# Kernel tuning notes

Hardware: AMD Instinct MI355X
Metric: run time of the kernel (lower is better)

The kernel has to match this reference:

```python
import jax, jax.numpy as jnp
import numpy as np

N, E, G = 50000, 600000, 50
IN_CH, HID, OUT, HEADS = 5, 64, 32, 4
BN_EPS = 1e-5


def setup_inputs() -> dict:
    key = jax.random.key(0)
    ks = jax.random.split(key, 32)

    def p(i, shape, scale=0.1):
        return jax.random.normal(ks[i], shape, dtype=jnp.float32) * scale

    inp = {
        "x": jax.random.normal(ks[0], (N, IN_CH), dtype=jnp.float32),
        "edge_index": jax.random.randint(ks[1], (2, E), 0, N),
        "batch": jnp.sort(jax.random.randint(ks[2], (N,), 0, G)),
        "enc_w": p(3, (IN_CH, HID)),
        "enc_b": jnp.zeros((HID,), jnp.float32),
    }
    dims = [(HID, HID), (HID, HID), (HID, OUT)]
    i = 4
    for l, (din, dout) in enumerate(dims):
        inp[f"w{l}"] = p(i, (din, HEADS * dout)); i += 1
        inp[f"as{l}"] = p(i, (HEADS, dout)); i += 1
        inp[f"ad{l}"] = p(i, (HEADS, dout)); i += 1
        inp[f"b{l}"] = jnp.zeros((dout,), jnp.float32)
        inp[f"g{l}"] = jnp.ones((dout,), jnp.float32)
        inp[f"be{l}"] = jnp.zeros((dout,), jnp.float32)
    for name in ("eth", "man"):
        inp[f"{name}_w1"] = p(i, (OUT, OUT // 2)); i += 1
        inp[f"{name}_b1"] = jnp.zeros((OUT // 2,), jnp.float32)
        inp[f"{name}_w2"] = p(i, (OUT // 2, 1)); i += 1
        inp[f"{name}_b2"] = jnp.zeros((1,), jnp.float32)
    return inp


def _gat(h_in, src, dst, W, a_s, a_d, bias, dout):
    # PyG GATConv, heads=HEADS, concat=False (mean over heads)
    h = (h_in @ W).reshape(N, HEADS, dout)          # [N,H,C]
    es = (h * a_s).sum(-1)                          # [N,H] src attention term
    ed = (h * a_d).sum(-1)                          # [N,H] dst attention term
    e = jax.nn.leaky_relu(es[src] + ed[dst], 0.2)   # [E,H]
    m = jax.ops.segment_max(e, dst, num_segments=N)
    ex = jnp.exp(e - m[dst])
    s = jax.ops.segment_sum(ex, dst, num_segments=N)
    alpha = ex / (s[dst] + 1e-16)                   # edge softmax per dst
    out = jax.ops.segment_sum(h[src] * alpha[..., None], dst, num_segments=N)
    return out.mean(axis=1) + bias                  # mean over heads + bias


def _bn(x, g, b):  # BatchNorm1d with batch statistics
    mu = x.mean(0)
    var = x.var(0)
    return g * (x - mu) * jax.lax.rsqrt(var + BN_EPS) + b


def _head(g, w1, b1, w2, b2):
    return jax.nn.sigmoid(jax.nn.relu(g @ w1 + b1) @ w2 + b2)


def reference(x, edge_index, batch, enc_w, enc_b,
              w0, as0, ad0, b0, g0, be0,
              w1, as1, ad1, b1, g1, be1,
              w2, as2, ad2, b2, g2, be2,
              eth_w1, eth_b1, eth_w2, eth_b2,
              man_w1, man_b1, man_w2, man_b2):
    loops = jnp.arange(N)
    src = jnp.concatenate([edge_index[0], loops])
    dst = jnp.concatenate([edge_index[1], loops])

    h = x @ enc_w + enc_b
    layers = [(w0, as0, ad0, b0, g0, be0, HID),
              (w1, as1, ad1, b1, g1, be1, HID),
              (w2, as2, ad2, b2, g2, be2, OUT)]
    for i, (W, a_s, a_d, bias, gm, bt, dout) in enumerate(layers):
        h = _gat(h, src, dst, W, a_s, a_d, bias, dout)
        h = _bn(h, gm, bt)
        if i < len(layers) - 1:
            h = jax.nn.relu(h)  # dropout is identity at inference

    ones = jnp.ones((N,), h.dtype)
    counts = jax.ops.segment_sum(ones, batch, num_segments=G)  # [G]
    gsum = jax.ops.segment_sum(h, batch, num_segments=G)
    gmean = gsum / jnp.maximum(counts, 1.0)[:, None]
    gmax = jax.ops.segment_max(h, batch, num_segments=G)
    gmax = jnp.where(counts[:, None] > 0, gmax, 0.0)
    gemb = (gmean + gmax + gsum) / 3.0

    ethics = _head(gemb, eth_w1, eth_b1, eth_w2, eth_b2)
    manip = _head(gemb, man_w1, man_b1, man_w2, man_b2)
    return h, gemb, ethics, manip
```

## Files before the change

kernel.cpp:

```cpp
#include <hip/hip_runtime.h>
#include <math.h>

constexpr int kN  = 50000;
constexpr int kE  = 600000;
constexpr int kET = 650000;
constexpr int kG  = 50;
constexpr int kH  = 4;
constexpr int kRep = 16;

constexpr size_t OFF_HCUR   = 0;
constexpr size_t OFF_HNEXT  = 1600000;
constexpr size_t OFF_Z      = 4800000;
constexpr size_t OFF_ES     = 11200000;
constexpr size_t OFF_ED     = 11400000;
constexpr size_t OFF_ROWPTR = 14200000;
constexpr size_t OFF_SRC    = 14320000;
constexpr size_t OFF_WT2    = 14970000;
constexpr size_t OFF_AHAT   = 15000000;
constexpr size_t OFF_SPART  = 15002000;
constexpr size_t OFF_CURSOR = 15010000;
constexpr size_t OFF_BNREP  = 15060000;
constexpr size_t OFF_GPOOL  = 15066144;
constexpr size_t kZeroEnd   = 15069344;

constexpr int kScanBlocks = (kN + 1023) / 1024;
constexpr int kHistBlocks = (kET + 255) / 256;
constexpr int kPrepBlocks = 163;
constexpr int kEncBlocks  = kN / 4;

typedef __bf16 bf16x8 __attribute__((ext_vector_type(8)));
typedef float  f32x4  __attribute__((ext_vector_type(4)));

__device__ inline ushort f2b(float f) {
    unsigned u = __float_as_uint(f);
    return (ushort)((u + 0x7FFFu + ((u >> 16) & 1u)) >> 16);
}
__device__ inline float b2f(ushort u) {
    return __uint_as_float(((unsigned)u) << 16);
}
__device__ inline unsigned enc_f(float f) {
    unsigned b = __float_as_uint(f);
    return (b & 0x80000000u) ? ~b : (b | 0x80000000u);
}
__device__ inline float dec_f(unsigned u) {
    return __uint_as_float((u & 0x80000000u) ? (u & 0x7FFFFFFFu) : ~u);
}

__device__ inline void edge_pair(const int* __restrict__ ei, int e, int& src, int& dst) {
    if (e < kE) { src = ei[e]; dst = ei[kE + e]; }
    else        { src = e - kE; dst = e - kE; }
}

__global__ void k_histprep(const int* __restrict__ ei, int* __restrict__ counts,
                           const float* __restrict__ w0, const float* __restrict__ w1,
                           const float* __restrict__ w2, const float* __restrict__ as0,
                           const float* __restrict__ as1, const float* __restrict__ as2,
                           const float* __restrict__ ad0, const float* __restrict__ ad1,
                           const float* __restrict__ ad2, float* __restrict__ ahat,
                           ushort* __restrict__ Wt2) {
    int b = blockIdx.x;
    if (b < 3) {
        const float* W  = (b == 0) ? w0 : (b == 1) ? w1 : w2;
        const float* As = (b == 0) ? as0 : (b == 1) ? as1 : as2;
        const float* Ad = (b == 0) ? ad0 : (b == 1) ? ad1 : ad2;
        int dout = (b == 2) ? 32 : 64;
        int i = threadIdx.x;
        int h = i >> 6, k = i & 63;
        const float* wr = W + (size_t)k * (4 * dout) + h * dout;
        float s1 = 0.f, s2 = 0.f;
        for (int c = 0; c < dout; ++c) {
            float w = wr[c];
            s1 += w * As[h * dout + c];
            s2 += w * Ad[h * dout + c];
        }
        ahat[b * 512 + i] = s1;
        ahat[b * 512 + 256 + i] = s2;
    } else if (b < kPrepBlocks) {
        int i = (b - 3) * 256 + threadIdx.x;
        if (i >= 40960) return;
        int l, li;
        if (i < 16384)      { l = 0; li = i; }
        else if (i < 32768) { l = 1; li = i - 16384; }
        else                { l = 2; li = i - 32768; }
        int dout = (l == 2) ? 32 : 64;
        const float* W = (l == 0) ? w0 : (l == 1) ? w1 : w2;
        int c = li >> 8, kk = li & 255;
        int h = kk >> 6, k = kk & 63;
        Wt2[l * 16384 + li] = f2b(W[(size_t)k * (4 * dout) + h * dout + c]);
    } else {
        int e = (b - kPrepBlocks) * 256 + threadIdx.x;
        if (e >= kET) return;
        int src, dst;
        edge_pair(ei, e, src, dst);
        atomicAdd(&counts[dst], 1);
    }
}

__global__ void __launch_bounds__(1024) k_scan_local(const int* __restrict__ counts,
                                                     int* __restrict__ rowptr,
                                                     int* __restrict__ partials) {
    int tid = threadIdx.x;
    int idx = blockIdx.x * 1024 + tid;
    int val = (idx < kN) ? counts[idx] : 0;
    int lane = tid & 63, w = tid >> 6;
    int x = val;
#pragma unroll
    for (int off = 1; off < 64; off <<= 1) {
        int t = __shfl_up(x, off);
        if (lane >= off) x += t;
    }
    __shared__ int wsum[16];
    if (lane == 63) wsum[w] = x;
    __syncthreads();
    if (w == 0 && lane < 16) {
        int y = wsum[lane];
#pragma unroll
        for (int off = 1; off < 16; off <<= 1) {
            int t = __shfl_up(y, off);
            if (lane >= off) y += t;
        }
        wsum[lane] = y;
    }
    __syncthreads();
    int incl = x + (w > 0 ? wsum[w - 1] : 0);
    if (idx < kN) rowptr[idx + 1] = incl;
    if (tid == 1023) partials[blockIdx.x] = incl;
}

__global__ void k_scan_part(int* __restrict__ partials) {
    int lane = threadIdx.x;
    int v = (lane < kScanBlocks) ? partials[lane] : 0;
    int x = v;
#pragma unroll
    for (int off = 1; off < 64; off <<= 1) {
        int t = __shfl_up(x, off);
        if (lane >= off) x += t;
    }
    if (lane < kScanBlocks) partials[lane] = x - v;
}

__global__ void __launch_bounds__(1024) k_scan_add(int* __restrict__ cursor,
                                                   int* __restrict__ rowptr,
                                                   const int* __restrict__ partials) {
    int idx = blockIdx.x * 1024 + threadIdx.x;
    if (idx >= kN) return;
    int incl = rowptr[idx + 1] + partials[blockIdx.x];
    rowptr[idx + 1] = incl;
    int val = cursor[idx];
    cursor[idx] = incl - val;
    if (idx == 0) rowptr[0] = 0;
}

__global__ void __launch_bounds__(256) k_scatter_enc(const int* __restrict__ ei,
                                                     int* __restrict__ cursor,
                                                     int* __restrict__ src_csr,
                                                     const float* __restrict__ x,
                                                     const float* __restrict__ w,
                                                     const float* __restrict__ b,
                                                     const float* __restrict__ ahat0,
                                                     ushort* __restrict__ h,
                                                     float* __restrict__ es,
                                                     float* __restrict__ ed) {
    if (blockIdx.x < kEncBlocks) {
        int node = blockIdx.x * 4 + (threadIdx.x >> 6);
        int lane = threadIdx.x & 63;
        float acc = b[lane];
#pragma unroll
        for (int k = 0; k < 5; ++k) acc += x[node * 5 + k] * w[k * 64 + lane];
        h[(size_t)node * 64 + lane] = f2b(acc);

        float ps[4], pd[4];
#pragma unroll
        for (int hh = 0; hh < 4; ++hh) {
            ps[hh] = acc * ahat0[hh * 64 + lane];
            pd[hh] = acc * ahat0[256 + hh * 64 + lane];
        }
#pragma unroll
        for (int off = 1; off < 64; off <<= 1) {
#pragma unroll
            for (int hh = 0; hh < 4; ++hh) {
                ps[hh] += __shfl_xor(ps[hh], off);
                pd[hh] += __shfl_xor(pd[hh], off);
            }
        }
        if (lane == 0) {
            ((float4*)es)[node] = make_float4(ps[0], ps[1], ps[2], ps[3]);
            ((float4*)ed)[node] = make_float4(pd[0], pd[1], pd[2], pd[3]);
        }
    } else {
        int e = (blockIdx.x - kEncBlocks) * 256 + threadIdx.x;
        if (e >= kET) return;
        int src, dst;
        edge_pair(ei, e, src, dst);
        int pos = atomicAdd(&cursor[dst], 1);
        src_csr[pos] = src;
    }
}

__global__ void __launch_bounds__(256) k_gat(const int* __restrict__ rowptr,
                                             const int* __restrict__ srcc,
                                             const float* __restrict__ es,
                                             const float* __restrict__ ed,
                                             const ushort* __restrict__ h,
                                             ushort* __restrict__ z) {
    int wid = threadIdx.x >> 6;
    int lane = threadIdx.x & 63;
    int dst = blockIdx.x * 4 + wid;
    int start = rowptr[dst], end = rowptr[dst + 1];
    int deg = end - start;

    int e_l = lane >> 2, hh = lane & 3;
    int q = lane >> 4, c4 = lane & 15;

    float edv = ed[dst * 4 + hh];
    float acc[4][4] = {};
    float s;

    if (deg <= 16) {
        int pos = start + e_l;
        int psafe = (pos < end) ? pos : start;
        int src = srcc[psafe];
        float v = es[src * 4 + hh] + edv;
        v = (v >= 0.f) ? v : 0.2f * v;
        if (pos >= end) v = -3e38f;

        uint2 hv[4];
#pragma unroll
        for (int t = 0; t < 4; ++t) {
            int p2 = start + t * 4 + q;
            int p2s = (p2 < end) ? p2 : start;
            int s2 = srcc[p2s];
            hv[t] = *reinterpret_cast<const uint2*>(h + (size_t)s2 * 64 + c4 * 4);
        }

        float cm = v;
        cm = fmaxf(cm, __shfl_xor(cm, 4));
        cm = fmaxf(cm, __shfl_xor(cm, 8));
        cm = fmaxf(cm, __shfl_xor(cm, 16));
        cm = fmaxf(cm, __shfl_xor(cm, 32));
        float p = __expf(v - cm);
        float cs = p;
        cs += __shfl_xor(cs, 4);
        cs += __shfl_xor(cs, 8);
        cs += __shfl_xor(cs, 16);
        cs += __shfl_xor(cs, 32);
        s = cs;

#pragma unroll
        for (int t = 0; t < 4; ++t) {
            int el = t * 4 + q;
            float p0 = __shfl(p, (el << 2) | 0);
            float p1 = __shfl(p, (el << 2) | 1);
            float p2 = __shfl(p, (el << 2) | 2);
            float p3 = __shfl(p, (el << 2) | 3);
            float c0 = __uint_as_float(hv[t].x << 16);
            float c1 = __uint_as_float(hv[t].x & 0xFFFF0000u);
            float c2 = __uint_as_float(hv[t].y << 16);
            float c3 = __uint_as_float(hv[t].y & 0xFFFF0000u);
            acc[0][0] += p0 * c0; acc[0][1] += p0 * c1; acc[0][2] += p0 * c2; acc[0][3] += p0 * c3;
            acc[1][0] += p1 * c0; acc[1][1] += p1 * c1; acc[1][2] += p1 * c2; acc[1][3] += p1 * c3;
            acc[2][0] += p2 * c0; acc[2][1] += p2 * c1; acc[2][2] += p2 * c2; acc[2][3] += p2 * c3;
            acc[3][0] += p3 * c0; acc[3][1] += p3 * c1; acc[3][2] += p3 * c2; acc[3][3] += p3 * c3;
        }
    } else {
        float m = -3e38f;
        s = 0.f;
        for (int cs0 = start; cs0 < end; cs0 += 16) {
            int pos = cs0 + e_l;
            int psafe = (pos < end) ? pos : start;
            int src = srcc[psafe];
            float v = es[src * 4 + hh] + edv;
            v = (v >= 0.f) ? v : 0.2f * v;
            if (pos >= end) v = -3e38f;

            float cm = v;
            cm = fmaxf(cm, __shfl_xor(cm, 4));
            cm = fmaxf(cm, __shfl_xor(cm, 8));
            cm = fmaxf(cm, __shfl_xor(cm, 16));
            cm = fmaxf(cm, __shfl_xor(cm, 32));
            float mn = fmaxf(m, cm);
            float scale = __expf(m - mn);
            float p = __expf(v - mn);
            float cth = p;
            cth += __shfl_xor(cth, 4);
            cth += __shfl_xor(cth, 8);
            cth += __shfl_xor(cth, 16);
            cth += __shfl_xor(cth, 32);
            s = s * scale + cth;
            m = mn;

            float sc0 = __shfl(scale, 0), sc1 = __shfl(scale, 1);
            float sc2 = __shfl(scale, 2), sc3 = __shfl(scale, 3);
#pragma unroll
            for (int c = 0; c < 4; ++c) {
                acc[0][c] *= sc0; acc[1][c] *= sc1; acc[2][c] *= sc2; acc[3][c] *= sc3;
            }
#pragma unroll
            for (int t = 0; t < 4; ++t) {
                int el = t * 4 + q;
                int p2 = cs0 + el;
                int p2s = (p2 < end) ? p2 : start;
                int s2 = srcc[p2s];
                uint2 hv = *reinterpret_cast<const uint2*>(h + (size_t)s2 * 64 + c4 * 4);
                float p0 = __shfl(p, (el << 2) | 0);
                float p1 = __shfl(p, (el << 2) | 1);
                float p2f = __shfl(p, (el << 2) | 2);
                float p3 = __shfl(p, (el << 2) | 3);
                float c0 = __uint_as_float(hv.x << 16);
                float c1 = __uint_as_float(hv.x & 0xFFFF0000u);
                float c2 = __uint_as_float(hv.y << 16);
                float c3 = __uint_as_float(hv.y & 0xFFFF0000u);
                acc[0][0] += p0 * c0;  acc[0][1] += p0 * c1;  acc[0][2] += p0 * c2;  acc[0][3] += p0 * c3;
                acc[1][0] += p1 * c0;  acc[1][1] += p1 * c1;  acc[1][2] += p1 * c2;  acc[1][3] += p1 * c3;
                acc[2][0] += p2f * c0; acc[2][1] += p2f * c1; acc[2][2] += p2f * c2; acc[2][3] += p2f * c3;
                acc[3][0] += p3 * c0;  acc[3][1] += p3 * c1;  acc[3][2] += p3 * c2;  acc[3][3] += p3 * c3;
            }
        }
    }

    float myinv = 0.25f / (s + 1e-16f);
    float inv0 = __shfl(myinv, 0), inv1 = __shfl(myinv, 1);
    float inv2 = __shfl(myinv, 2), inv3 = __shfl(myinv, 3);
#pragma unroll
    for (int c = 0; c < 4; ++c) {
        acc[0][c] *= inv0; acc[1][c] *= inv1; acc[2][c] *= inv2; acc[3][c] *= inv3;
    }
#pragma unroll
    for (int j = 0; j < 4; ++j) {
#pragma unroll
        for (int c = 0; c < 4; ++c) {
            float v = acc[j][c];
            v += __shfl_xor(v, 16);
            v += __shfl_xor(v, 32);
            acc[j][c] = v;
        }
    }
    if (q == 0) {
        ushort* zr = z + (size_t)dst * 256 + c4 * 4;
#pragma unroll
        for (int j = 0; j < 4; ++j) {
            ushort4 o;
            o.x = f2b(acc[j][0]); o.y = f2b(acc[j][1]);
            o.z = f2b(acc[j][2]); o.w = f2b(acc[j][3]);
            *reinterpret_cast<ushort4*>(zr + j * 64) = o;
        }
    }
}

template <int DOUT>
__global__ void __launch_bounds__(256) k_zgemm(const ushort* __restrict__ z,
                                               const ushort* __restrict__ Wt2l,
                                               float* __restrict__ hnext,
                                               float* __restrict__ bnrep_l) {
    constexpr int NT = DOUT / 16;
    constexpr int W = 2 * DOUT;
    __shared__ float pl[4][W];
    int tid = threadIdx.x;
    int widx = tid >> 6, lane = tid & 63;
    int wid = blockIdx.x * 4 + widx;
    int mtile = wid / NT;
    int nt = wid - mtile * NT;
    bool active = (mtile < kN / 16);
    int m0 = mtile * 16;
    int n0 = nt * 16;

    int row = lane & 15;
    int k0  = (lane >> 4) * 8;

    for (int j = tid; j < 4 * W; j += 256) (&pl[0][0])[j] = 0.f;

    f32x4 acc = {0.f, 0.f, 0.f, 0.f};
    if (active) {
        const ushort* za = z + (size_t)(m0 + row) * 256 + k0;
        const ushort* wb = Wt2l + (size_t)(n0 + row) * 256 + k0;
#pragma unroll
        for (int ks = 0; ks < 8; ++ks) {
            bf16x8 a = *reinterpret_cast<const bf16x8*>(za + ks * 32);
            bf16x8 b = *reinterpret_cast<const bf16x8*>(wb + ks * 32);
            acc = __builtin_amdgcn_mfma_f32_16x16x32_bf16(a, b, acc, 0, 0, 0);
        }
        int col = lane & 15;
        int r0  = (lane >> 4) * 4;
#pragma unroll
        for (int r = 0; r < 4; ++r)
            hnext[(size_t)(m0 + r0 + r) * DOUT + n0 + col] = acc[r];
    }

    float s0 = 0.f, q0 = 0.f;
#pragma unroll
    for (int r = 0; r < 4; ++r) { s0 += acc[r]; q0 += acc[r] * acc[r]; }
    s0 += __shfl_xor(s0, 16); s0 += __shfl_xor(s0, 32);
    q0 += __shfl_xor(q0, 16); q0 += __shfl_xor(q0, 32);
    __syncthreads();
    if (lane < 16) {
        pl[widx][n0 + lane]        = s0;
        pl[widx][DOUT + n0 + lane] = q0;
    }
    __syncthreads();
    if (tid < W) {
        float t = pl[0][tid] + pl[1][tid] + pl[2][tid] + pl[3][tid];
        atomicAdd(&bnrep_l[(blockIdx.x & (kRep - 1)) * 128 + tid], t);
    }
}

__global__ void __launch_bounds__(256) k_bn_apply_att(const float* __restrict__ hnext,
                                                      const float* __restrict__ bnrep_l,
                                                      const float* __restrict__ g,
                                                      const float* __restrict__ be,
                                                      const float* __restrict__ ahat_next,
                                                      ushort* __restrict__ hcur,
                                                      float* __restrict__ es,
                                                      float* __restrict__ ed) {
    int node = blockIdx.x * 4 + (threadIdx.x >> 6);
    int lane = threadIdx.x & 63;
    float bs = 0.f, bq = 0.f;
#pragma unroll
    for (int r = 0; r < kRep; ++r) {
        bs += bnrep_l[r * 128 + lane];
        bq += bnrep_l[r * 128 + 64 + lane];
    }
    float mu = bs * (1.f / kN);
    float var = bq * (1.f / kN) - mu * mu;
    float v = g[lane] * (hnext[(size_t)node * 64 + lane] - mu) * rsqrtf(var + 1e-5f) + be[lane];
    v = fmaxf(v, 0.f);
    hcur[(size_t)node * 64 + lane] = f2b(v);

    float ps[4], pd[4];
#pragma unroll
    for (int hh = 0; hh < 4; ++hh) {
        ps[hh] = v * ahat_next[hh * 64 + lane];
        pd[hh] = v * ahat_next[256 + hh * 64 + lane];
    }
#pragma unroll
    for (int off = 1; off < 64; off <<= 1) {
#pragma unroll
        for (int hh = 0; hh < 4; ++hh) {
            ps[hh] += __shfl_xor(ps[hh], off);
            pd[hh] += __shfl_xor(pd[hh], off);
        }
    }
    if (lane == 0) {
        ((float4*)es)[node] = make_float4(ps[0], ps[1], ps[2], ps[3]);
        ((float4*)ed)[node] = make_float4(pd[0], pd[1], pd[2], pd[3]);
    }
}

__global__ void __launch_bounds__(256) k_bn_apply32_pool(const float* __restrict__ hnext,
                                                         const float* __restrict__ bnrep_l,
                                                         const float* __restrict__ g,
                                                         const float* __restrict__ be,
                                                         const int* __restrict__ batch,
                                                         float* __restrict__ out_h,
                                                         float* __restrict__ gsum,
                                                         unsigned* __restrict__ gmaxe) {
    int tid = threadIdx.x;
    int i = blockIdx.x * 256 + tid;
    int n = i >> 5, c = i & 31;
    float bs = 0.f, bq = 0.f;
#pragma unroll
    for (int r = 0; r < kRep; ++r) {
        bs += bnrep_l[r * 128 + c];
        bq += bnrep_l[r * 128 + 32 + c];
    }
    float mu = bs * (1.f / kN);
    float var = bq * (1.f / kN) - mu * mu;
    float v = g[c] * (hnext[i] - mu) * rsqrtf(var + 1e-5f) + be[c];
    out_h[i] = v;

    __shared__ float ls[256];
    ls[tid] = v;
    __syncthreads();
    int nb0 = blockIdx.x * 8;
    int gfirst = batch[nb0], glast = batch[nb0 + 7];
    if (gfirst == glast) {
        if (tid < 32) {
            float s = 0.f;
            unsigned me = 0u;
#pragma unroll
            for (int r = 0; r < 8; ++r) {
                float vv = ls[r * 32 + tid];
                s += vv;
                unsigned e = enc_f(vv);
                me = (e > me) ? e : me;
            }
            atomicAdd(&gsum[gfirst * 32 + tid], s);
            atomicMax(&gmaxe[gfirst * 32 + tid], me);
        }
    } else {
        int gg = batch[n];
        atomicAdd(&gsum[gg * 32 + c], v);
        atomicMax(&gmaxe[gg * 32 + c], enc_f(v));
    }
}

__global__ void __launch_bounds__(256) k_finish(const float* __restrict__ gsum,
                                                const unsigned* __restrict__ gmaxe,
                                                const int* __restrict__ batch,
                                                const float* __restrict__ ew1,
                                                const float* __restrict__ eb1,
                                                const float* __restrict__ ew2,
                                                const float* __restrict__ eb2,
                                                const float* __restrict__ mw1,
                                                const float* __restrict__ mb1,
                                                const float* __restrict__ mw2,
                                                const float* __restrict__ mb2,
                                                float* __restrict__ out_gemb,
                                                float* __restrict__ out_eth,
                                                float* __restrict__ out_man) {
    __shared__ int bound[kG + 1];
    __shared__ float ge[kG * 32];
    int tid = threadIdx.x;
    if (tid <= kG) {
        int lo = 0, hi = kN;
        while (lo < hi) { int mid = (lo + hi) >> 1; if (batch[mid] < tid) lo = mid + 1; else hi = mid; }
        bound[tid] = lo;
    }
    __syncthreads();
    for (int j = tid; j < kG * 32; j += 256) {
        int gg = j >> 5;
        int cnt = bound[gg + 1] - bound[gg];
        float sum = gsum[j];
        float mx = (cnt > 0) ? dec_f(gmaxe[j]) : 0.f;
        float mean = sum / fmaxf((float)cnt, 1.f);
        float e = (mean + mx + sum) * (1.f / 3.f);
        ge[j] = e;
        out_gemb[j] = e;
    }
    __syncthreads();
    if (tid < kG) {
        const float* row = &ge[tid * 32];
        float acc_e = eb2[0], acc_m = mb2[0];
#pragma unroll 4
        for (int j = 0; j < 16; ++j) {
            float he = eb1[j], hm = mb1[j];
            for (int k = 0; k < 32; ++k) {
                float v = row[k];
                he += v * ew1[k * 16 + j];
                hm += v * mw1[k * 16 + j];
            }
            acc_e += fmaxf(he, 0.f) * ew2[j];
            acc_m += fmaxf(hm, 0.f) * mw2[j];
        }
        out_eth[tid] = 1.f / (1.f + expf(-acc_e));
        out_man[tid] = 1.f / (1.f + expf(-acc_m));
    }
}

extern "C" void kernel_launch(void* const* d_in, const int* in_sizes, int n_in,
                              void* d_out, int out_size, void* d_ws, size_t ws_size,
                              hipStream_t stream) {
    const float* x     = (const float*)d_in[0];
    const int*   ei    = (const int*)d_in[1];
    const int*   batch = (const int*)d_in[2];
    const float* enc_w = (const float*)d_in[3];
    const float* enc_b = (const float*)d_in[4];

    float* ws = (float*)d_ws;
    ushort*   hcur  = (ushort*)(ws + OFF_HCUR);
    float*    hnext = ws + OFF_HNEXT;
    ushort*   z     = (ushort*)(ws + OFF_Z);
    float*    es    = ws + OFF_ES;
    float*    ed    = ws + OFF_ED;
    int*      rowptr= (int*)(ws + OFF_ROWPTR);
    int*      srcc  = (int*)(ws + OFF_SRC);
    ushort*   Wt2   = (ushort*)(ws + OFF_WT2);
    float*    ahat  = ws + OFF_AHAT;
    int*      spart = (int*)(ws + OFF_SPART);
    int*      cursor= (int*)(ws + OFF_CURSOR);
    float*    bnrep = ws + OFF_BNREP;
    float*    gsum  = ws + OFF_GPOOL;
    unsigned* gmaxe = (unsigned*)(ws + OFF_GPOOL + 1600);

    float* out      = (float*)d_out;
    float* out_h    = out;
    float* out_gemb = out + 1600000;
    float* out_eth  = out + 1601600;
    float* out_man  = out + 1601650;

    hipMemsetAsync(ws + OFF_CURSOR, 0, (kZeroEnd - OFF_CURSOR) * sizeof(float), stream);

    k_histprep<<<kPrepBlocks + kHistBlocks, 256, 0, stream>>>(
        ei, cursor,
        (const float*)d_in[5], (const float*)d_in[11], (const float*)d_in[17],
        (const float*)d_in[6], (const float*)d_in[12], (const float*)d_in[18],
        (const float*)d_in[7], (const float*)d_in[13], (const float*)d_in[19],
        ahat, Wt2);

    k_scan_local<<<kScanBlocks, 1024, 0, stream>>>(cursor, rowptr, spart);
    k_scan_part<<<1, 64, 0, stream>>>(spart);
    k_scan_add<<<kScanBlocks, 1024, 0, stream>>>(cursor, rowptr, spart);

    k_scatter_enc<<<kEncBlocks + kHistBlocks, 256, 0, stream>>>(
        ei, cursor, srcc, x, enc_w, enc_b, ahat, hcur, es, ed);

    for (int l = 0; l < 3; ++l) {
        const float* gam = (const float*)d_in[9 + 6 * l];
        const float* bet = (const float*)d_in[10 + 6 * l];
        const ushort* Wt2l = Wt2 + l * 16384;
        float* bnrep_l = bnrep + l * kRep * 128;

        k_gat<<<kN / 4, 256, 0, stream>>>(rowptr, srcc, es, ed, hcur, z);

        if (l < 2) {
            k_zgemm<64><<<3125, 256, 0, stream>>>(z, Wt2l, hnext, bnrep_l);
            k_bn_apply_att<<<kN / 4, 256, 0, stream>>>(hnext, bnrep_l, gam, bet,
                                                       ahat + (l + 1) * 512, hcur, es, ed);
        } else {
            k_zgemm<32><<<1563, 256, 0, stream>>>(z, Wt2l, hnext, bnrep_l);
            k_bn_apply32_pool<<<kN * 32 / 256, 256, 0, stream>>>(hnext, bnrep_l, gam, bet,
                                                                 batch, out_h, gsum, gmaxe);
        }
    }

    k_finish<<<1, 256, 0, stream>>>(gsum, gmaxe, batch,
                                    (const float*)d_in[23], (const float*)d_in[24],
                                    (const float*)d_in[25], (const float*)d_in[26],
                                    (const float*)d_in[27], (const float*)d_in[28],
                                    (const float*)d_in[29], (const float*)d_in[30],
                                    out_gemb, out_eth, out_man);
}
```

Before: 488.0 us.

## Fuse GAT aggregation with projection GEMM via LDS and place self-loops directly

The per-destination attention aggregation now writes its 16 rows of bf16 head features into shared memory, and the same 1024-thread block runs the MFMA projection and BN partial sums. This removes the global round trip for the intermediate z buffer and one kernel launch per layer. Separately, the CSR scatter now handles four edges per thread, and each self-loop is written directly to the last slot of its row instead of going through an atomic. In exchange, the larger blocks lower scheduling flexibility, and most waves sit idle during the small GEMM phase.

```diff
diff --git a/kernel.cpp b/kernel.cpp
--- a/kernel.cpp
+++ b/kernel.cpp
@@ -10,7 +10,6 @@
 
 constexpr size_t OFF_HCUR   = 0;
 constexpr size_t OFF_HNEXT  = 1600000;
-constexpr size_t OFF_Z      = 4800000;
 constexpr size_t OFF_ES     = 11200000;
 constexpr size_t OFF_ED     = 11400000;
 constexpr size_t OFF_ROWPTR = 14200000;
@@ -27,6 +26,8 @@
 constexpr int kHistBlocks = (kET + 255) / 256;
 constexpr int kPrepBlocks = 163;
 constexpr int kEncBlocks  = kN / 4;
+constexpr int kSctBlocks  = (kE / 4 + 255) / 256;
+constexpr int kLoopBlocks = (kN + 255) / 256;
 
 typedef __bf16 bf16x8 __attribute__((ext_vector_type(8)));
 typedef float  f32x4  __attribute__((ext_vector_type(4)));
@@ -154,6 +155,7 @@
 __global__ void __launch_bounds__(256) k_scatter_enc(const int* __restrict__ ei,
                                                      int* __restrict__ cursor,
                                                      int* __restrict__ src_csr,
+                                                     const int* __restrict__ rowptr,
                                                      const float* __restrict__ x,
                                                      const float* __restrict__ w,
                                                      const float* __restrict__ b,
@@ -187,25 +189,46 @@
             ((float4*)es)[node] = make_float4(ps[0], ps[1], ps[2], ps[3]);
             ((float4*)ed)[node] = make_float4(pd[0], pd[1], pd[2], pd[3]);
         }
+    } else if (blockIdx.x < kEncBlocks + kSctBlocks) {
+        int e0 = ((blockIdx.x - kEncBlocks) * 256 + threadIdx.x) * 4;
+        int srcv[4], dstv[4];
+#pragma unroll
+        for (int u = 0; u < 4; ++u) {
+            int e = e0 + u;
+            if (e < kE) { srcv[u] = ei[e]; dstv[u] = ei[kE + e]; }
+            else        { srcv[u] = -1; }
+        }
+#pragma unroll
+        for (int u = 0; u < 4; ++u) {
+            if (srcv[u] >= 0) {
+                int pos = atomicAdd(&cursor[dstv[u]], 1);
+                src_csr[pos] = srcv[u];
+            }
+        }
     } else {
-        int e = (blockIdx.x - kEncBlocks) * 256 + threadIdx.x;
-        if (e >= kET) return;
-        int src, dst;
-        edge_pair(ei, e, src, dst);
-        int pos = atomicAdd(&cursor[dst], 1);
-        src_csr[pos] = src;
-    }
-}
-
-__global__ void __launch_bounds__(256) k_gat(const int* __restrict__ rowptr,
-                                             const int* __restrict__ srcc,
-                                             const float* __restrict__ es,
-                                             const float* __restrict__ ed,
-                                             const ushort* __restrict__ h,
-                                             ushort* __restrict__ z) {
-    int wid = threadIdx.x >> 6;
-    int lane = threadIdx.x & 63;
-    int dst = blockIdx.x * 4 + wid;
+        int d = (blockIdx.x - kEncBlocks - kSctBlocks) * 256 + threadIdx.x;
+        if (d >= kN) return;
+        src_csr[rowptr[d + 1] - 1] = d;
+    }
+}
+
+template <int DOUT>
+__global__ void __launch_bounds__(1024) k_gatgemm(const int* __restrict__ rowptr,
+                                                  const int* __restrict__ srcc,
+                                                  const float* __restrict__ es,
+                                                  const float* __restrict__ ed,
+                                                  const ushort* __restrict__ h,
+                                                  const ushort* __restrict__ Wt2l,
+                                                  float* __restrict__ hnext,
+                                                  float* __restrict__ bnrep_l) {
+    constexpr int NT = DOUT / 16;
+    constexpr int W = 2 * DOUT;
+    __shared__ ushort zl[16][264];
+    __shared__ float bnp[W];
+
+    int tid = threadIdx.x;
+    int w = tid >> 6, lane = tid & 63;
+    int dst = blockIdx.x * 16 + w;
     int start = rowptr[dst], end = rowptr[dst + 1];
     int deg = end - start;
 
@@ -336,7 +359,7 @@
         }
     }
     if (q == 0) {
-        ushort* zr = z + (size_t)dst * 256 + c4 * 4;
+        ushort* zr = &zl[w][c4 * 4];
 #pragma unroll
         for (int j = 0; j < 4; ++j) {
             ushort4 o;
@@ -345,61 +368,40 @@
             *reinterpret_cast<ushort4*>(zr + j * 64) = o;
         }
     }
-}
-
-template <int DOUT>
-__global__ void __launch_bounds__(256) k_zgemm(const ushort* __restrict__ z,
-                                               const ushort* __restrict__ Wt2l,
-                                               float* __restrict__ hnext,
-                                               float* __restrict__ bnrep_l) {
-    constexpr int NT = DOUT / 16;
-    constexpr int W = 2 * DOUT;
-    __shared__ float pl[4][W];
-    int tid = threadIdx.x;
-    int widx = tid >> 6, lane = tid & 63;
-    int wid = blockIdx.x * 4 + widx;
-    int mtile = wid / NT;
-    int nt = wid - mtile * NT;
-    bool active = (mtile < kN / 16);
-    int m0 = mtile * 16;
-    int n0 = nt * 16;
-
-    int row = lane & 15;
-    int k0  = (lane >> 4) * 8;
-
-    for (int j = tid; j < 4 * W; j += 256) (&pl[0][0])[j] = 0.f;
-
-    f32x4 acc = {0.f, 0.f, 0.f, 0.f};
-    if (active) {
-        const ushort* za = z + (size_t)(m0 + row) * 256 + k0;
-        const ushort* wb = Wt2l + (size_t)(n0 + row) * 256 + k0;
+    __syncthreads();
+
+    f32x4 gacc = {0.f, 0.f, 0.f, 0.f};
+    if (w < NT) {
+        int row = lane & 15;
+        int k0  = (lane >> 4) * 8;
+        const ushort* za = &zl[row][k0];
+        const ushort* wb = Wt2l + (size_t)(w * 16 + row) * 256 + k0;
 #pragma unroll
         for (int ks = 0; ks < 8; ++ks) {
             bf16x8 a = *reinterpret_cast<const bf16x8*>(za + ks * 32);
-            bf16x8 b = *reinterpret_cast<const bf16x8*>(wb + ks * 32);
-            acc = __builtin_amdgcn_mfma_f32_16x16x32_bf16(a, b, acc, 0, 0, 0);
+            bf16x8 bb = *reinterpret_cast<const bf16x8*>(wb + ks * 32);
+            gacc = __builtin_amdgcn_mfma_f32_16x16x32_bf16(a, bb, gacc, 0, 0, 0);
         }
         int col = lane & 15;
         int r0  = (lane >> 4) * 4;
+        int m0  = blockIdx.x * 16;
 #pragma unroll
         for (int r = 0; r < 4; ++r)
-            hnext[(size_t)(m0 + r0 + r) * DOUT + n0 + col] = acc[r];
-    }
-
-    float s0 = 0.f, q0 = 0.f;
-#pragma unroll
-    for (int r = 0; r < 4; ++r) { s0 += acc[r]; q0 += acc[r] * acc[r]; }
-    s0 += __shfl_xor(s0, 16); s0 += __shfl_xor(s0, 32);
-    q0 += __shfl_xor(q0, 16); q0 += __shfl_xor(q0, 32);
-    __syncthreads();
-    if (lane < 16) {
-        pl[widx][n0 + lane]        = s0;
-        pl[widx][DOUT + n0 + lane] = q0;
+            hnext[(size_t)(m0 + r0 + r) * DOUT + w * 16 + col] = gacc[r];
+
+        float s0 = 0.f, q0 = 0.f;
+#pragma unroll
+        for (int r = 0; r < 4; ++r) { s0 += gacc[r]; q0 += gacc[r] * gacc[r]; }
+        s0 += __shfl_xor(s0, 16); s0 += __shfl_xor(s0, 32);
+        q0 += __shfl_xor(q0, 16); q0 += __shfl_xor(q0, 32);
+        if (lane < 16) {
+            bnp[w * 16 + lane]        = s0;
+            bnp[DOUT + w * 16 + lane] = q0;
+        }
     }
     __syncthreads();
     if (tid < W) {
-        float t = pl[0][tid] + pl[1][tid] + pl[2][tid] + pl[3][tid];
-        atomicAdd(&bnrep_l[(blockIdx.x & (kRep - 1)) * 128 + tid], t);
+        atomicAdd(&bnrep_l[(blockIdx.x & (kRep - 1)) * 128 + tid], bnp[tid]);
     }
 }
 
@@ -558,7 +560,6 @@
     float* ws = (float*)d_ws;
     ushort*   hcur  = (ushort*)(ws + OFF_HCUR);
     float*    hnext = ws + OFF_HNEXT;
-    ushort*   z     = (ushort*)(ws + OFF_Z);
     float*    es    = ws + OFF_ES;
     float*    ed    = ws + OFF_ED;
     int*      rowptr= (int*)(ws + OFF_ROWPTR);
@@ -590,8 +591,8 @@
     k_scan_part<<<1, 64, 0, stream>>>(spart);
     k_scan_add<<<kScanBlocks, 1024, 0, stream>>>(cursor, rowptr, spart);
 
-    k_scatter_enc<<<kEncBlocks + kHistBlocks, 256, 0, stream>>>(
-        ei, cursor, srcc, x, enc_w, enc_b, ahat, hcur, es, ed);
+    k_scatter_enc<<<kEncBlocks + kSctBlocks + kLoopBlocks, 256, 0, stream>>>(
+        ei, cursor, srcc, rowptr, x, enc_w, enc_b, ahat, hcur, es, ed);
 
     for (int l = 0; l < 3; ++l) {
         const float* gam = (const float*)d_in[9 + 6 * l];
@@ -599,14 +600,14 @@
         const ushort* Wt2l = Wt2 + l * 16384;
         float* bnrep_l = bnrep + l * kRep * 128;
 
-        k_gat<<<kN / 4, 256, 0, stream>>>(rowptr, srcc, es, ed, hcur, z);
-
         if (l < 2) {
-            k_zgemm<64><<<3125, 256, 0, stream>>>(z, Wt2l, hnext, bnrep_l);
+            k_gatgemm<64><<<kN / 16, 1024, 0, stream>>>(rowptr, srcc, es, ed, hcur,
+                                                        Wt2l, hnext, bnrep_l);
             k_bn_apply_att<<<kN / 4, 256, 0, stream>>>(hnext, bnrep_l, gam, bet,
                                                        ahat + (l + 1) * 512, hcur, es, ed);
         } else {
-            k_zgemm<32><<<1563, 256, 0, stream>>>(z, Wt2l, hnext, bnrep_l);
+            k_gatgemm<32><<<kN / 16, 1024, 0, stream>>>(rowptr, srcc, es, ed, hcur,
+                                                        Wt2l, hnext, bnrep_l);
             k_bn_apply32_pool<<<kN * 32 / 256, 256, 0, stream>>>(hnext, bnrep_l, gam, bet,
                                                                  batch, out_h, gsum, gmaxe);
         }
```

Measured after the change: 516.6 us. 1.06x slower.

## Use 16-bit CSR source indices and range-partitioned scatter with appended self-loops

Applied to the files above, without the earlier changes.

CSR source indices are now stored as 16-bit values, which fit because N is below 65536. This halves index traffic in the CSR build and in every GAT layer's neighbour gather. The edge scatter is split into eight destination ranges, each handled by its own set of blocks that read edges four at a time with vector loads, so the atomic cursor updates and CSR writes land in a smaller address window. Self-loops are no longer scattered through atomics; they are written directly into the last slot of each row. In exchange, the edge list is read eight times, and the code relies on N fitting in 16 bits.

```diff
diff --git a/kernel.cpp b/kernel.cpp
--- a/kernel.cpp
+++ b/kernel.cpp
@@ -7,6 +7,7 @@
 constexpr int kG  = 50;
 constexpr int kH  = 4;
 constexpr int kRep = 16;
+constexpr int kRangeSz = 6250;
 
 constexpr size_t OFF_HCUR   = 0;
 constexpr size_t OFF_HNEXT  = 1600000;
@@ -27,6 +28,9 @@
 constexpr int kHistBlocks = (kET + 255) / 256;
 constexpr int kPrepBlocks = 163;
 constexpr int kEncBlocks  = kN / 4;
+constexpr int kChunks     = (kE + 1023) / 1024;
+constexpr int kSctBlocks  = kChunks * 8;
+constexpr int kLoopBlocks = (kN + 255) / 256;
 
 typedef __bf16 bf16x8 __attribute__((ext_vector_type(8)));
 typedef float  f32x4  __attribute__((ext_vector_type(4)));
@@ -153,7 +157,8 @@
 
 __global__ void __launch_bounds__(256) k_scatter_enc(const int* __restrict__ ei,
                                                      int* __restrict__ cursor,
-                                                     int* __restrict__ src_csr,
+                                                     ushort* __restrict__ src_csr,
+                                                     const int* __restrict__ rowptr,
                                                      const float* __restrict__ x,
                                                      const float* __restrict__ w,
                                                      const float* __restrict__ b,
@@ -187,18 +192,33 @@
             ((float4*)es)[node] = make_float4(ps[0], ps[1], ps[2], ps[3]);
             ((float4*)ed)[node] = make_float4(pd[0], pd[1], pd[2], pd[3]);
         }
+    } else if (blockIdx.x < kEncBlocks + kSctBlocks) {
+        int bs = blockIdx.x - kEncBlocks;
+        int chunk = bs >> 3;
+        int range = blockIdx.x & 7;
+        int dlo = range * kRangeSz;
+        int e0 = (chunk * 256 + threadIdx.x) * 4;
+        if (e0 >= kE) return;
+        int4 dv = *reinterpret_cast<const int4*>(ei + kE + e0);
+        int4 sv = *reinterpret_cast<const int4*>(ei + e0);
+        int dstv[4] = {dv.x, dv.y, dv.z, dv.w};
+        int srcv[4] = {sv.x, sv.y, sv.z, sv.w};
+#pragma unroll
+        for (int u = 0; u < 4; ++u) {
+            if (e0 + u < kE && (unsigned)(dstv[u] - dlo) < (unsigned)kRangeSz) {
+                int pos = atomicAdd(&cursor[dstv[u]], 1);
+                src_csr[pos] = (ushort)srcv[u];
+            }
+        }
     } else {
-        int e = (blockIdx.x - kEncBlocks) * 256 + threadIdx.x;
-        if (e >= kET) return;
-        int src, dst;
-        edge_pair(ei, e, src, dst);
-        int pos = atomicAdd(&cursor[dst], 1);
-        src_csr[pos] = src;
+        int d = (blockIdx.x - kEncBlocks - kSctBlocks) * 256 + threadIdx.x;
+        if (d >= kN) return;
+        src_csr[rowptr[d + 1] - 1] = (ushort)d;
     }
 }
 
 __global__ void __launch_bounds__(256) k_gat(const int* __restrict__ rowptr,
-                                             const int* __restrict__ srcc,
+                                             const ushort* __restrict__ srcc,
                                              const float* __restrict__ es,
                                              const float* __restrict__ ed,
                                              const ushort* __restrict__ h,
@@ -562,7 +582,7 @@
     float*    es    = ws + OFF_ES;
     float*    ed    = ws + OFF_ED;
     int*      rowptr= (int*)(ws + OFF_ROWPTR);
-    int*      srcc  = (int*)(ws + OFF_SRC);
+    ushort*   srcc  = (ushort*)(ws + OFF_SRC);
     ushort*   Wt2   = (ushort*)(ws + OFF_WT2);
     float*    ahat  = ws + OFF_AHAT;
     int*      spart = (int*)(ws + OFF_SPART);
@@ -590,8 +610,8 @@
     k_scan_part<<<1, 64, 0, stream>>>(spart);
     k_scan_add<<<kScanBlocks, 1024, 0, stream>>>(cursor, rowptr, spart);
 
-    k_scatter_enc<<<kEncBlocks + kHistBlocks, 256, 0, stream>>>(
-        ei, cursor, srcc, x, enc_w, enc_b, ahat, hcur, es, ed);
+    k_scatter_enc<<<kEncBlocks + kSctBlocks + kLoopBlocks, 256, 0, stream>>>(
+        ei, cursor, srcc, rowptr, x, enc_w, enc_b, ahat, hcur, es, ed);
 
     for (int l = 0; l < 3; ++l) {
         const float* gam = (const float*)d_in[9 + 6 * l];
```

Result: faster. 473.7 us (-2.9%).
